# Optimization experiments

Measured on AMD Instinct MI355X. Metric: run time of the kernel, lower is better.

The kernel has to match this reference:

```python
import jax, jax.numpy as jnp
import numpy as np

B, T, D, H = 4, 2048, 1024, 2048   # batch, seq, d_model, moe_dim
E, S, K = 8, 2, 2                   # routed experts, shared experts, top_k


def setup_inputs() -> dict:
    key = jax.random.key(0)
    ks = jax.random.split(key, 10)
    s = 0.02  # init scale
    return {
        "x": jax.random.normal(ks[0], (B, T, D), jnp.float32),
        "gate_w": jax.random.normal(ks[1], (D, E), jnp.float32) * s,
        "gate_b": jnp.zeros((E,), jnp.float32),
        # routed experts, stacked over expert axis
        "rw1": jax.random.normal(ks[2], (E, D, H), jnp.float32) * s,
        "rb1": jnp.zeros((E, H), jnp.float32),
        "rw2": jax.random.normal(ks[3], (E, D, H), jnp.float32) * s,
        "rb2": jnp.zeros((E, H), jnp.float32),
        "rw3": jax.random.normal(ks[4], (E, H, D), jnp.float32) * s,
        "rb3": jnp.zeros((E, D), jnp.float32),
        # shared experts, stacked
        "sw1": jax.random.normal(ks[5], (S, D, H), jnp.float32) * s,
        "sb1": jnp.zeros((S, H), jnp.float32),
        "sw2": jax.random.normal(ks[6], (S, D, H), jnp.float32) * s,
        "sb2": jnp.zeros((S, H), jnp.float32),
        "sw3": jax.random.normal(ks[7], (S, H, D), jnp.float32) * s,
        "sb3": jnp.zeros((S, D), jnp.float32),
    }


def _swiglu_stacked(x, w1, b1, w2, b2, w3, b3):
    # x: (B,T,D); w1/w2: (N,D,H); w3: (N,H,D) -> out: (N,B,T,D)
    p1 = jnp.einsum('btd,ndh->nbth', x, w1) + b1[:, None, None, :]
    p2 = jnp.einsum('btd,ndh->nbth', x, w2) + b2[:, None, None, :]
    glu = jax.nn.silu(p1) * p2
    return jnp.einsum('nbth,nhd->nbtd', glu, w3) + b3[:, None, None, :]


def reference(x, gate_w, gate_b, rw1, rb1, rw2, rb2, rw3, rb3,
              sw1, sb1, sw2, sb2, sw3, sb3):
    # Gate: softmax over all routed experts, then top-k (no renormalization)
    scores = jax.nn.softmax(x @ gate_w + gate_b, axis=-1)      # (B,T,E)
    weights, indices = jax.lax.top_k(scores, K)                # (B,T,K)

    # Routed experts: compute all experts densely (same math as the naive
    # masked-dense torch loop), then gather top-k outputs per token.
    routed_all = _swiglu_stacked(x, rw1, rb1, rw2, rb2, rw3, rb3)  # (E,B,T,D)
    out_bted = jnp.transpose(routed_all, (1, 2, 0, 3))             # (B,T,E,D)
    gathered = jnp.take_along_axis(out_bted, indices[..., None], axis=2)  # (B,T,K,D)
    routed = jnp.sum(weights[..., None] * gathered, axis=2)        # (B,T,D)

    # Shared experts: mean over shared experts
    shared = _swiglu_stacked(x, sw1, sb1, sw2, sb2, sw3, sb3).mean(axis=0)

    return shared + routed
```

## Files before the change

kernel.cpp:

```cpp
#include <hip/hip_runtime.h>
#include <math.h>

#define TOKENS   8192
#define DMODEL   1024
#define HDIM     2048
#define NEXP     8
#define NSH      2
#define NGRP     10
#define R_ROUTED 16384
#define R_TOTAL  32768

typedef float  f32x4  __attribute__((ext_vector_type(4)));
typedef __bf16 bf16x8 __attribute__((ext_vector_type(8)));
typedef unsigned short u16x8 __attribute__((ext_vector_type(8)));

typedef __attribute__((address_space(1))) const void as1_void;
typedef __attribute__((address_space(3))) void as3_void;
#define GLOAD16(g, l) __builtin_amdgcn_global_load_lds((as1_void*)(g), (as3_void*)(l), 16, 0, 0)

__device__ __forceinline__ unsigned short f2bf(float f) {
  unsigned int u = __float_as_uint(f);
  u += 0x7fffu + ((u >> 16) & 1u);
  return (unsigned short)(u >> 16);
}
__device__ __forceinline__ float bf2f(unsigned short u) {
  return __uint_as_float(((unsigned int)u) << 16);
}


__global__ __launch_bounds__(256) void convert_x_kernel(const float* __restrict__ x,
                                                        unsigned short* __restrict__ xb) {
  int i = blockIdx.x * blockDim.x + threadIdx.x;
  const float4 v = reinterpret_cast<const float4*>(x)[i];
  ushort4 o;
  o.x = f2bf(v.x); o.y = f2bf(v.y); o.z = f2bf(v.z); o.w = f2bf(v.w);
  reinterpret_cast<ushort4*>(xb)[i] = o;
}

__global__ __launch_bounds__(256) void transpose_cvt64_kernel(const float* __restrict__ src,
                                                              unsigned short* __restrict__ dst,
                                                              int R, int C) {
  __shared__ float tile[64][65];
  const size_t mat = blockIdx.z;
  src += mat * (size_t)R * C;
  dst += mat * (size_t)R * C;
  const int c0 = blockIdx.x * 64, r0 = blockIdx.y * 64;
  const int tid = threadIdx.x;
  const int tx = tid & 15, ty = tid >> 4;
  #pragma unroll
  for (int rr = 0; rr < 4; ++rr) {
    const int row = ty + rr * 16;
    const float4 v = *reinterpret_cast<const float4*>(&src[(size_t)(r0 + row) * C + c0 + tx * 4]);
    tile[row][tx * 4 + 0] = v.x;
    tile[row][tx * 4 + 1] = v.y;
    tile[row][tx * 4 + 2] = v.z;
    tile[row][tx * 4 + 3] = v.w;
  }
  __syncthreads();
  const int oc = tid >> 2, og = tid & 3;
  u16x8 u0, u1;
  #pragma unroll
  for (int e = 0; e < 8; ++e) u0[e] = f2bf(tile[og * 16 + e][oc]);
  #pragma unroll
  for (int e = 0; e < 8; ++e) u1[e] = f2bf(tile[og * 16 + 8 + e][oc]);
  unsigned short* dp = &dst[(size_t)(c0 + oc) * R + r0 + og * 16];
  *reinterpret_cast<u16x8*>(dp) = u0;
  *reinterpret_cast<u16x8*>(dp + 8) = u1;
}


__global__ __launch_bounds__(64) void gate_kernel(const float* __restrict__ x,
                                                  const float* __restrict__ gw,
                                                  const float* __restrict__ gb,
                                                  int* __restrict__ topk_idx,
                                                  float* __restrict__ topk_w,
                                                  int* __restrict__ counts) {
  const int t = blockIdx.x;
  const int lane = threadIdx.x;
  const float* xr = x + (size_t)t * DMODEL;
  float acc[NEXP];
  #pragma unroll
  for (int e = 0; e < NEXP; ++e) acc[e] = 0.f;
  for (int d = lane; d < DMODEL; d += 64) {
    const float xv = xr[d];
    const float* g = gw + (size_t)d * NEXP;
    #pragma unroll
    for (int e = 0; e < NEXP; ++e) acc[e] += xv * g[e];
  }
  #pragma unroll
  for (int e = 0; e < NEXP; ++e) {
    float v = acc[e];
    v += __shfl_down(v, 32); v += __shfl_down(v, 16); v += __shfl_down(v, 8);
    v += __shfl_down(v, 4);  v += __shfl_down(v, 2);  v += __shfl_down(v, 1);
    acc[e] = v;
  }
  if (lane == 0) {
    float p[NEXP];
    float mx = -1e30f;
    #pragma unroll
    for (int e = 0; e < NEXP; ++e) { acc[e] += gb[e]; mx = fmaxf(mx, acc[e]); }
    float s = 0.f;
    #pragma unroll
    for (int e = 0; e < NEXP; ++e) { p[e] = expf(acc[e] - mx); s += p[e]; }
    const float inv = 1.f / s;
    #pragma unroll
    for (int e = 0; e < NEXP; ++e) p[e] *= inv;
    int i1 = 0; float v1 = p[0];
    #pragma unroll
    for (int e = 1; e < NEXP; ++e) if (p[e] > v1) { v1 = p[e]; i1 = e; }
    int i2 = -1; float v2 = -1e30f;
    #pragma unroll
    for (int e = 0; e < NEXP; ++e) if (e != i1 && p[e] > v2) { v2 = p[e]; i2 = e; }
    topk_idx[t * 2 + 0] = i1; topk_w[t * 2 + 0] = v1;
    topk_idx[t * 2 + 1] = i2; topk_w[t * 2 + 1] = v2;
    atomicAdd(&counts[i1], 1);
    atomicAdd(&counts[i2], 1);
  }
}

__global__ void offs_kernel(const int* __restrict__ counts, int* __restrict__ offs) {
  if (threadIdx.x == 0 && blockIdx.x == 0) {
    int cum = 0;
    for (int e = 0; e < NEXP; ++e) { offs[e] = cum; cum += counts[e]; }
    offs[8] = R_ROUTED;
    offs[9] = R_ROUTED + TOKENS;
    offs[10] = R_TOTAL;
  }
}

__global__ __launch_bounds__(256) void scatter_kernel(const int* __restrict__ topk_idx,
                                                      const int* __restrict__ offs,
                                                      int* __restrict__ cursors,
                                                      int* __restrict__ row_token,
                                                      int* __restrict__ tok_rows) {
  const int t = blockIdx.x * blockDim.x + threadIdx.x;
  if (t >= TOKENS) return;
  #pragma unroll
  for (int k = 0; k < 2; ++k) {
    const int e = topk_idx[t * 2 + k];
    const int pos = atomicAdd(&cursors[e], 1);
    const int r = offs[e] + pos;
    row_token[r] = t;
    tok_rows[t * 2 + k] = r;
  }
  row_token[R_ROUTED + t] = t;
  row_token[R_ROUTED + TOKENS + t] = t;
}


__global__ __launch_bounds__(256, 3) void gemm1_kernel(
    const unsigned short* __restrict__ xb,
    const unsigned short* __restrict__ w1t,
    const unsigned short* __restrict__ w2t,
    const float* __restrict__ rb1, const float* __restrict__ sb1,
    const float* __restrict__ rb2, const float* __restrict__ sb2,
    const int* __restrict__ offs,
    const int* __restrict__ row_token,
    unsigned short* __restrict__ glu) {
  const int g = blockIdx.z;
  const int off_g = offs[g];
  const int n_g = offs[g + 1] - off_g;
  const int m0 = blockIdx.x * 128;
  if (m0 >= n_g) return;
  const int n0 = blockIdx.y * 64;

  __shared__ __align__(16) unsigned short Abuf[128 * 64];
  __shared__ __align__(16) unsigned short B1buf[64 * 64];
  __shared__ __align__(16) unsigned short B2buf[64 * 64];

  const int tid = threadIdx.x;
  const int lane = tid & 63;
  const int wid = tid >> 6;
  const int wm = wid >> 1, wn = wid & 1;
  const int l15 = lane & 15, kq = lane >> 4;

  const unsigned short* w1g = w1t + (size_t)g * HDIM * DMODEL;
  const unsigned short* w2g = w2t + (size_t)g * HDIM * DMODEL;

  const unsigned short* srcA[4]; int dA[4];
  #pragma unroll
  for (int r = 0; r < 4; ++r) {
    const int chunk = r * 256 + tid, row = chunk >> 3, j = chunk & 7;
    int ar = m0 + row; if (ar > n_g - 1) ar = n_g - 1;
    srcA[r] = xb + (size_t)row_token[off_g + ar] * DMODEL + ((j ^ (row & 7)) << 3);
    dA[r] = (r * 256 + (tid & ~63)) << 3;
  }
  const unsigned short* srcB1[2]; const unsigned short* srcB2[2]; int dB[2];
  #pragma unroll
  for (int r = 0; r < 2; ++r) {
    const int chunk = r * 256 + tid, row = chunk >> 3, j = chunk & 7;
    const size_t o = (size_t)(n0 + row) * DMODEL + ((j ^ (row & 7)) << 3);
    srcB1[r] = w1g + o; srcB2[r] = w2g + o;
    dB[r] = (r * 256 + (tid & ~63)) << 3;
  }

  f32x4 acc1[4][2], acc2[4][2];
  const f32x4 zero = {0.f, 0.f, 0.f, 0.f};
  #pragma unroll
  for (int i = 0; i < 4; ++i)
    #pragma unroll
    for (int j = 0; j < 2; ++j) { acc1[i][j] = zero; acc2[i][j] = zero; }

  for (int k0 = 0; k0 < DMODEL; k0 += 64) {
    __syncthreads();
    #pragma unroll
    for (int r = 0; r < 4; ++r) GLOAD16(srcA[r] + k0, &Abuf[dA[r]]);
    #pragma unroll
    for (int r = 0; r < 2; ++r) {
      GLOAD16(srcB1[r] + k0, &B1buf[dB[r]]);
      GLOAD16(srcB2[r] + k0, &B2buf[dB[r]]);
    }
    __syncthreads();
    #pragma unroll
    for (int ks = 0; ks < 2; ++ks) {
      const int kc = ks * 4 + kq;
      bf16x8 a[4], p[2], q[2];
      #pragma unroll
      for (int mi = 0; mi < 4; ++mi) {
        const int row = wm * 64 + mi * 16 + l15;
        a[mi] = *reinterpret_cast<const bf16x8*>(&Abuf[row * 64 + ((kc ^ (row & 7)) << 3)]);
      }
      #pragma unroll
      for (int ni = 0; ni < 2; ++ni) {
        const int row = wn * 32 + ni * 16 + l15;
        const int ko = (kc ^ (row & 7)) << 3;
        p[ni] = *reinterpret_cast<const bf16x8*>(&B1buf[row * 64 + ko]);
        q[ni] = *reinterpret_cast<const bf16x8*>(&B2buf[row * 64 + ko]);
      }
      #pragma unroll
      for (int mi = 0; mi < 4; ++mi)
        #pragma unroll
        for (int ni = 0; ni < 2; ++ni) {
          acc1[mi][ni] = __builtin_amdgcn_mfma_f32_16x16x32_bf16(a[mi], p[ni], acc1[mi][ni], 0, 0, 0);
          acc2[mi][ni] = __builtin_amdgcn_mfma_f32_16x16x32_bf16(a[mi], q[ni], acc2[mi][ni], 0, 0, 0);
        }
    }
  }

  const float* b1p = (g < NEXP) ? (rb1 + (size_t)g * HDIM) : (sb1 + (size_t)(g - NEXP) * HDIM);
  const float* b2p = (g < NEXP) ? (rb2 + (size_t)g * HDIM) : (sb2 + (size_t)(g - NEXP) * HDIM);

  #pragma unroll
  for (int mi = 0; mi < 4; ++mi) {
    #pragma unroll
    for (int r = 0; r < 4; ++r) {
      const int m = m0 + wm * 64 + mi * 16 + kq * 4 + r;
      if (m < n_g) {
        #pragma unroll
        for (int ni = 0; ni < 2; ++ni) {
          const int n = n0 + wn * 32 + ni * 16 + l15;
          const float x1 = acc1[mi][ni][r] + b1p[n];
          const float x2 = acc2[mi][ni][r] + b2p[n];
          glu[(size_t)(off_g + m) * HDIM + n] = f2bf((x1 / (1.f + expf(-x1))) * x2);
        }
      }
    }
  }
}


__global__ __launch_bounds__(256, 3) void gemm2_kernel(
    const unsigned short* __restrict__ glu,
    const unsigned short* __restrict__ w3t,
    const float* __restrict__ rb3, const float* __restrict__ sb3,
    const int* __restrict__ offs,
    unsigned short* __restrict__ y) {
  const int g = blockIdx.z;
  const int off_g = offs[g];
  const int n_g = offs[g + 1] - off_g;
  const int m0 = blockIdx.x * 128;
  if (m0 >= n_g) return;
  const int n0 = blockIdx.y * 128;

  __shared__ __align__(16) unsigned short Abuf[128 * 64];
  __shared__ __align__(16) unsigned short Bbuf[128 * 64];

  const int tid = threadIdx.x;
  const int lane = tid & 63;
  const int wid = tid >> 6;
  const int wm = wid >> 1, wn = wid & 1;
  const int l15 = lane & 15, kq = lane >> 4;

  const unsigned short* w3g = w3t + (size_t)g * DMODEL * HDIM;

  const unsigned short* srcA[4]; const unsigned short* srcB[4]; int dAB[4];
  #pragma unroll
  for (int r = 0; r < 4; ++r) {
    const int chunk = r * 256 + tid, row = chunk >> 3, j = chunk & 7;
    int ar = m0 + row; if (ar > n_g - 1) ar = n_g - 1;
    srcA[r] = glu + (size_t)(off_g + ar) * HDIM + ((j ^ (row & 7)) << 3);
    srcB[r] = w3g + (size_t)(n0 + row) * HDIM + ((j ^ (row & 7)) << 3);
    dAB[r] = (r * 256 + (tid & ~63)) << 3;
  }

  f32x4 acc[4][4];
  const f32x4 zero = {0.f, 0.f, 0.f, 0.f};
  #pragma unroll
  for (int i = 0; i < 4; ++i)
    #pragma unroll
    for (int j = 0; j < 4; ++j) acc[i][j] = zero;

  for (int k0 = 0; k0 < HDIM; k0 += 64) {
    __syncthreads();
    #pragma unroll
    for (int r = 0; r < 4; ++r) {
      GLOAD16(srcA[r] + k0, &Abuf[dAB[r]]);
      GLOAD16(srcB[r] + k0, &Bbuf[dAB[r]]);
    }
    __syncthreads();
    #pragma unroll
    for (int ks = 0; ks < 2; ++ks) {
      const int kc = ks * 4 + kq;
      bf16x8 a[4], b[4];
      #pragma unroll
      for (int mi = 0; mi < 4; ++mi) {
        const int row = wm * 64 + mi * 16 + l15;
        a[mi] = *reinterpret_cast<const bf16x8*>(&Abuf[row * 64 + ((kc ^ (row & 7)) << 3)]);
      }
      #pragma unroll
      for (int ni = 0; ni < 4; ++ni) {
        const int row = wn * 64 + ni * 16 + l15;
        b[ni] = *reinterpret_cast<const bf16x8*>(&Bbuf[row * 64 + ((kc ^ (row & 7)) << 3)]);
      }
      #pragma unroll
      for (int mi = 0; mi < 4; ++mi)
        #pragma unroll
        for (int ni = 0; ni < 4; ++ni)
          acc[mi][ni] = __builtin_amdgcn_mfma_f32_16x16x32_bf16(a[mi], b[ni], acc[mi][ni], 0, 0, 0);
    }
  }

  const float* b3p = (g < NEXP) ? (rb3 + (size_t)g * DMODEL) : (sb3 + (size_t)(g - NEXP) * DMODEL);

  #pragma unroll
  for (int mi = 0; mi < 4; ++mi) {
    #pragma unroll
    for (int r = 0; r < 4; ++r) {
      const int m = m0 + wm * 64 + mi * 16 + kq * 4 + r;
      if (m < n_g) {
        unsigned short* yrow = y + (size_t)(off_g + m) * DMODEL;
        #pragma unroll
        for (int ni = 0; ni < 4; ++ni) {
          const int n = n0 + wn * 64 + ni * 16 + l15;
          yrow[n] = f2bf(acc[mi][ni][r] + b3p[n]);
        }
      }
    }
  }
}


__global__ __launch_bounds__(256) void reduce_kernel(const unsigned short* __restrict__ y,
                                                     const int* __restrict__ tok_rows,
                                                     const float* __restrict__ topk_w,
                                                     float* __restrict__ out) {
  const int t = blockIdx.x * 2 + (threadIdx.x >> 7);
  const int col = (threadIdx.x & 127) * 8;
  const int r0 = tok_rows[t * 2 + 0], r1 = tok_rows[t * 2 + 1];
  const float w0 = topk_w[t * 2 + 0], w1 = topk_w[t * 2 + 1];

  float o[8];
  #pragma unroll
  for (int e = 0; e < 8; ++e) o[e] = 0.f;
  auto addrow = [&](const unsigned short* p, float w) {
    const u16x8 v = *reinterpret_cast<const u16x8*>(p);
    #pragma unroll
    for (int e = 0; e < 8; ++e) o[e] += w * bf2f(v[e]);
  };
  addrow(y + (size_t)r0 * DMODEL + col, w0);
  addrow(y + (size_t)r1 * DMODEL + col, w1);
  addrow(y + (size_t)(R_ROUTED + t) * DMODEL + col, 0.5f);
  addrow(y + (size_t)(R_ROUTED + TOKENS + t) * DMODEL + col, 0.5f);

  float4* op = reinterpret_cast<float4*>(out + (size_t)t * DMODEL + col);
  op[0] = make_float4(o[0], o[1], o[2], o[3]);
  op[1] = make_float4(o[4], o[5], o[6], o[7]);
}


extern "C" void kernel_launch(void* const* d_in, const int* in_sizes, int n_in,
                              void* d_out, int out_size, void* d_ws, size_t ws_size,
                              hipStream_t stream) {
  const float* x      = (const float*)d_in[0];
  const float* gate_w = (const float*)d_in[1];
  const float* gate_b = (const float*)d_in[2];
  const float* rw1    = (const float*)d_in[3];
  const float* rb1    = (const float*)d_in[4];
  const float* rw2    = (const float*)d_in[5];
  const float* rb2    = (const float*)d_in[6];
  const float* rw3    = (const float*)d_in[7];
  const float* rb3    = (const float*)d_in[8];
  const float* sw1    = (const float*)d_in[9];
  const float* sb1    = (const float*)d_in[10];
  const float* sw2    = (const float*)d_in[11];
  const float* sb2    = (const float*)d_in[12];
  const float* sw3    = (const float*)d_in[13];
  const float* sb3    = (const float*)d_in[14];
  float* out = (float*)d_out;

  const size_t XB_OFF   = 0;
  const size_t W1T_OFF  = XB_OFF  + (size_t)TOKENS * DMODEL * 2;
  const size_t W2T_OFF  = W1T_OFF + (size_t)NGRP * HDIM * DMODEL * 2;
  const size_t W3T_OFF  = W2T_OFF + (size_t)NGRP * HDIM * DMODEL * 2;
  const size_t GLU_OFF  = W3T_OFF + (size_t)NGRP * DMODEL * HDIM * 2;
  const size_t Y_OFF    = W1T_OFF;
  const size_t RTOK_OFF = GLU_OFF + (size_t)R_TOTAL * HDIM * 2;
  const size_t TKI_OFF  = RTOK_OFF + (size_t)R_TOTAL * 4;
  const size_t TKW_OFF  = TKI_OFF + (size_t)TOKENS * 2 * 4;
  const size_t TRW_OFF  = TKW_OFF + (size_t)TOKENS * 2 * 4;
  const size_t META_OFF = TRW_OFF + (size_t)TOKENS * 2 * 4;
  const size_t NEED     = META_OFF + 256;
  if (ws_size < NEED) return;

  char* ws = (char*)d_ws;
  unsigned short* xb   = (unsigned short*)(ws + XB_OFF);
  unsigned short* w1t  = (unsigned short*)(ws + W1T_OFF);
  unsigned short* w2t  = (unsigned short*)(ws + W2T_OFF);
  unsigned short* w3t  = (unsigned short*)(ws + W3T_OFF);
  unsigned short* glu  = (unsigned short*)(ws + GLU_OFF);
  unsigned short* yy   = (unsigned short*)(ws + Y_OFF);
  int*   row_token = (int*)(ws + RTOK_OFF);
  int*   topk_idx  = (int*)(ws + TKI_OFF);
  float* topk_w    = (float*)(ws + TKW_OFF);
  int*   tok_rows  = (int*)(ws + TRW_OFF);
  int*   counts    = (int*)(ws + META_OFF);
  int*   offs      = counts + 16;
  int*   cursors   = counts + 32;

  hipMemsetAsync(counts, 0, 192, stream);

  convert_x_kernel<<<TOKENS * DMODEL / 4 / 256, 256, 0, stream>>>(x, xb);

  transpose_cvt64_kernel<<<dim3(HDIM / 64, DMODEL / 64, NEXP), 256, 0, stream>>>(rw1, w1t, DMODEL, HDIM);
  transpose_cvt64_kernel<<<dim3(HDIM / 64, DMODEL / 64, NSH), 256, 0, stream>>>(
      sw1, w1t + (size_t)NEXP * HDIM * DMODEL, DMODEL, HDIM);
  transpose_cvt64_kernel<<<dim3(HDIM / 64, DMODEL / 64, NEXP), 256, 0, stream>>>(rw2, w2t, DMODEL, HDIM);
  transpose_cvt64_kernel<<<dim3(HDIM / 64, DMODEL / 64, NSH), 256, 0, stream>>>(
      sw2, w2t + (size_t)NEXP * HDIM * DMODEL, DMODEL, HDIM);
  transpose_cvt64_kernel<<<dim3(DMODEL / 64, HDIM / 64, NEXP), 256, 0, stream>>>(rw3, w3t, HDIM, DMODEL);
  transpose_cvt64_kernel<<<dim3(DMODEL / 64, HDIM / 64, NSH), 256, 0, stream>>>(
      sw3, w3t + (size_t)NEXP * DMODEL * HDIM, HDIM, DMODEL);

  gate_kernel<<<TOKENS, 64, 0, stream>>>(x, gate_w, gate_b, topk_idx, topk_w, counts);
  offs_kernel<<<1, 64, 0, stream>>>(counts, offs);
  scatter_kernel<<<TOKENS / 256, 256, 0, stream>>>(topk_idx, offs, cursors,
                                                   row_token, tok_rows);

  gemm1_kernel<<<dim3(TOKENS / 128, HDIM / 64, NGRP), 256, 0, stream>>>(
      xb, w1t, w2t, rb1, sb1, rb2, sb2, offs, row_token, glu);
  gemm2_kernel<<<dim3(TOKENS / 128, DMODEL / 128, NGRP), 256, 0, stream>>>(
      glu, w3t, rb3, sb3, offs, yy);
  reduce_kernel<<<TOKENS / 2, 256, 0, stream>>>(yy, tok_rows, topk_w, out);
}
```

Measured before the change: 1.040 ms.

## Merge weight-transpose launches, fuse x conversion into gate, use 8-wave GEMM blocks

```diff
diff --git a/kernel.cpp b/kernel.cpp
--- a/kernel.cpp
+++ b/kernel.cpp
@@ -27,23 +27,20 @@
   return __uint_as_float(((unsigned int)u) << 16);
 }
 
-
-__global__ __launch_bounds__(256) void convert_x_kernel(const float* __restrict__ x,
-                                                        unsigned short* __restrict__ xb) {
-  int i = blockIdx.x * blockDim.x + threadIdx.x;
-  const float4 v = reinterpret_cast<const float4*>(x)[i];
-  ushort4 o;
-  o.x = f2bf(v.x); o.y = f2bf(v.y); o.z = f2bf(v.z); o.w = f2bf(v.w);
-  reinterpret_cast<ushort4*>(xb)[i] = o;
-}
-
-__global__ __launch_bounds__(256) void transpose_cvt64_kernel(const float* __restrict__ src,
-                                                              unsigned short* __restrict__ dst,
-                                                              int R, int C) {
+__global__ __launch_bounds__(256) void transpose_cvt64_kernel(
+    const float* __restrict__ s0, const float* __restrict__ s1,
+    const float* __restrict__ s2, const float* __restrict__ s3,
+    unsigned short* __restrict__ dst, int R, int C, int n0, int n1) {
   __shared__ float tile[64][65];
-  const size_t mat = blockIdx.z;
-  src += mat * (size_t)R * C;
-  dst += mat * (size_t)R * C;
+  const int z = blockIdx.z;
+  const size_t msz = (size_t)R * C;
+  const float* src;
+  if (z < n0) src = s0 + (size_t)z * msz;
+  else if (z < n0 + n1) src = s1 + (size_t)(z - n0) * msz;
+  else if (z < n0 + n1 + 8) src = s2 + (size_t)(z - n0 - n1) * msz;
+  else src = s3 + (size_t)(z - n0 - n1 - 8) * msz;
+  unsigned short* d = dst + (size_t)z * msz;
+
   const int c0 = blockIdx.x * 64, r0 = blockIdx.y * 64;
   const int tid = threadIdx.x;
   const int tx = tid & 15, ty = tid >> 4;
@@ -63,29 +60,40 @@
   for (int e = 0; e < 8; ++e) u0[e] = f2bf(tile[og * 16 + e][oc]);
   #pragma unroll
   for (int e = 0; e < 8; ++e) u1[e] = f2bf(tile[og * 16 + 8 + e][oc]);
-  unsigned short* dp = &dst[(size_t)(c0 + oc) * R + r0 + og * 16];
+  unsigned short* dp = &d[(size_t)(c0 + oc) * R + r0 + og * 16];
   *reinterpret_cast<u16x8*>(dp) = u0;
   *reinterpret_cast<u16x8*>(dp + 8) = u1;
 }
 
 
-__global__ __launch_bounds__(64) void gate_kernel(const float* __restrict__ x,
-                                                  const float* __restrict__ gw,
-                                                  const float* __restrict__ gb,
-                                                  int* __restrict__ topk_idx,
-                                                  float* __restrict__ topk_w,
-                                                  int* __restrict__ counts) {
-  const int t = blockIdx.x;
-  const int lane = threadIdx.x;
+__global__ __launch_bounds__(256) void gate_kernel(const float* __restrict__ x,
+                                                   const float* __restrict__ gw,
+                                                   const float* __restrict__ gb,
+                                                   int* __restrict__ topk_idx,
+                                                   float* __restrict__ topk_w,
+                                                   int* __restrict__ counts,
+                                                   unsigned short* __restrict__ xb) {
+  const int t = blockIdx.x * 4 + (threadIdx.x >> 6);
+  const int lane = threadIdx.x & 63;
   const float* xr = x + (size_t)t * DMODEL;
+  unsigned short* xbr = xb + (size_t)t * DMODEL;
   float acc[NEXP];
   #pragma unroll
   for (int e = 0; e < NEXP; ++e) acc[e] = 0.f;
-  for (int d = lane; d < DMODEL; d += 64) {
-    const float xv = xr[d];
-    const float* g = gw + (size_t)d * NEXP;
-    #pragma unroll
-    for (int e = 0; e < NEXP; ++e) acc[e] += xv * g[e];
+  #pragma unroll
+  for (int j = 0; j < 4; ++j) {
+    const int d = j * 256 + lane * 4;
+    const float4 v = *reinterpret_cast<const float4*>(&xr[d]);
+    ushort4 o;
+    o.x = f2bf(v.x); o.y = f2bf(v.y); o.z = f2bf(v.z); o.w = f2bf(v.w);
+    *reinterpret_cast<ushort4*>(&xbr[d]) = o;
+    #pragma unroll
+    for (int q = 0; q < 4; ++q) {
+      const float xv = (&v.x)[q];
+      const float* g = gw + (size_t)(d + q) * NEXP;
+      #pragma unroll
+      for (int e = 0; e < NEXP; ++e) acc[e] += xv * g[e];
+    }
   }
   #pragma unroll
   for (int e = 0; e < NEXP; ++e) {
@@ -148,7 +156,7 @@
 }
 
 
-__global__ __launch_bounds__(256, 3) void gemm1_kernel(
+__global__ __launch_bounds__(512, 4) void gemm1_kernel(
     const unsigned short* __restrict__ xb,
     const unsigned short* __restrict__ w1t,
     const unsigned short* __restrict__ w2t,
@@ -171,95 +179,84 @@
   const int tid = threadIdx.x;
   const int lane = tid & 63;
   const int wid = tid >> 6;
-  const int wm = wid >> 1, wn = wid & 1;
+  const int wm = wid >> 2, wn = wid & 3;
   const int l15 = lane & 15, kq = lane >> 4;
 
   const unsigned short* w1g = w1t + (size_t)g * HDIM * DMODEL;
   const unsigned short* w2g = w2t + (size_t)g * HDIM * DMODEL;
 
-  const unsigned short* srcA[4]; int dA[4];
-  #pragma unroll
-  for (int r = 0; r < 4; ++r) {
-    const int chunk = r * 256 + tid, row = chunk >> 3, j = chunk & 7;
+  const unsigned short* srcA[2]; int dA[2];
+  #pragma unroll
+  for (int r = 0; r < 2; ++r) {
+    const int chunk = r * 512 + tid, row = chunk >> 3, j = chunk & 7;
     int ar = m0 + row; if (ar > n_g - 1) ar = n_g - 1;
     srcA[r] = xb + (size_t)row_token[off_g + ar] * DMODEL + ((j ^ (row & 7)) << 3);
-    dA[r] = (r * 256 + (tid & ~63)) << 3;
-  }
-  const unsigned short* srcB1[2]; const unsigned short* srcB2[2]; int dB[2];
-  #pragma unroll
-  for (int r = 0; r < 2; ++r) {
-    const int chunk = r * 256 + tid, row = chunk >> 3, j = chunk & 7;
+    dA[r] = (r * 512 + (tid & ~63)) << 3;
+  }
+  const unsigned short* srcB1; const unsigned short* srcB2; int dB;
+  {
+    const int row = tid >> 3, j = tid & 7;
     const size_t o = (size_t)(n0 + row) * DMODEL + ((j ^ (row & 7)) << 3);
-    srcB1[r] = w1g + o; srcB2[r] = w2g + o;
-    dB[r] = (r * 256 + (tid & ~63)) << 3;
-  }
-
-  f32x4 acc1[4][2], acc2[4][2];
+    srcB1 = w1g + o; srcB2 = w2g + o;
+    dB = (tid & ~63) << 3;
+  }
+
+  f32x4 acc1[4], acc2[4];
   const f32x4 zero = {0.f, 0.f, 0.f, 0.f};
   #pragma unroll
-  for (int i = 0; i < 4; ++i)
-    #pragma unroll
-    for (int j = 0; j < 2; ++j) { acc1[i][j] = zero; acc2[i][j] = zero; }
+  for (int i = 0; i < 4; ++i) { acc1[i] = zero; acc2[i] = zero; }
 
   for (int k0 = 0; k0 < DMODEL; k0 += 64) {
     __syncthreads();
-    #pragma unroll
-    for (int r = 0; r < 4; ++r) GLOAD16(srcA[r] + k0, &Abuf[dA[r]]);
-    #pragma unroll
-    for (int r = 0; r < 2; ++r) {
-      GLOAD16(srcB1[r] + k0, &B1buf[dB[r]]);
-      GLOAD16(srcB2[r] + k0, &B2buf[dB[r]]);
-    }
+    GLOAD16(srcA[0] + k0, &Abuf[dA[0]]);
+    GLOAD16(srcA[1] + k0, &Abuf[dA[1]]);
+    GLOAD16(srcB1 + k0, &B1buf[dB]);
+    GLOAD16(srcB2 + k0, &B2buf[dB]);
     __syncthreads();
     #pragma unroll
     for (int ks = 0; ks < 2; ++ks) {
       const int kc = ks * 4 + kq;
-      bf16x8 a[4], p[2], q[2];
+      bf16x8 a[4], p, q;
       #pragma unroll
       for (int mi = 0; mi < 4; ++mi) {
         const int row = wm * 64 + mi * 16 + l15;
         a[mi] = *reinterpret_cast<const bf16x8*>(&Abuf[row * 64 + ((kc ^ (row & 7)) << 3)]);
       }
-      #pragma unroll
-      for (int ni = 0; ni < 2; ++ni) {
-        const int row = wn * 32 + ni * 16 + l15;
+      {
+        const int row = wn * 16 + l15;
         const int ko = (kc ^ (row & 7)) << 3;
-        p[ni] = *reinterpret_cast<const bf16x8*>(&B1buf[row * 64 + ko]);
-        q[ni] = *reinterpret_cast<const bf16x8*>(&B2buf[row * 64 + ko]);
-      }
-      #pragma unroll
-      for (int mi = 0; mi < 4; ++mi)
-        #pragma unroll
-        for (int ni = 0; ni < 2; ++ni) {
-          acc1[mi][ni] = __builtin_amdgcn_mfma_f32_16x16x32_bf16(a[mi], p[ni], acc1[mi][ni], 0, 0, 0);
-          acc2[mi][ni] = __builtin_amdgcn_mfma_f32_16x16x32_bf16(a[mi], q[ni], acc2[mi][ni], 0, 0, 0);
-        }
+        p = *reinterpret_cast<const bf16x8*>(&B1buf[row * 64 + ko]);
+        q = *reinterpret_cast<const bf16x8*>(&B2buf[row * 64 + ko]);
+      }
+      #pragma unroll
+      for (int mi = 0; mi < 4; ++mi) {
+        acc1[mi] = __builtin_amdgcn_mfma_f32_16x16x32_bf16(a[mi], p, acc1[mi], 0, 0, 0);
+        acc2[mi] = __builtin_amdgcn_mfma_f32_16x16x32_bf16(a[mi], q, acc2[mi], 0, 0, 0);
+      }
     }
   }
 
   const float* b1p = (g < NEXP) ? (rb1 + (size_t)g * HDIM) : (sb1 + (size_t)(g - NEXP) * HDIM);
   const float* b2p = (g < NEXP) ? (rb2 + (size_t)g * HDIM) : (sb2 + (size_t)(g - NEXP) * HDIM);
 
+  const int n = n0 + wn * 16 + l15;
+  const float bb1 = b1p[n], bb2 = b2p[n];
   #pragma unroll
   for (int mi = 0; mi < 4; ++mi) {
     #pragma unroll
     for (int r = 0; r < 4; ++r) {
       const int m = m0 + wm * 64 + mi * 16 + kq * 4 + r;
       if (m < n_g) {
-        #pragma unroll
-        for (int ni = 0; ni < 2; ++ni) {
-          const int n = n0 + wn * 32 + ni * 16 + l15;
-          const float x1 = acc1[mi][ni][r] + b1p[n];
-          const float x2 = acc2[mi][ni][r] + b2p[n];
-          glu[(size_t)(off_g + m) * HDIM + n] = f2bf((x1 / (1.f + expf(-x1))) * x2);
-        }
+        const float x1 = acc1[mi][r] + bb1;
+        const float x2 = acc2[mi][r] + bb2;
+        glu[(size_t)(off_g + m) * HDIM + n] = f2bf((x1 / (1.f + expf(-x1))) * x2);
       }
     }
   }
 }
 
 
-__global__ __launch_bounds__(256, 3) void gemm2_kernel(
+__global__ __launch_bounds__(512, 4) void gemm2_kernel(
     const unsigned short* __restrict__ glu,
     const unsigned short* __restrict__ w3t,
     const float* __restrict__ rb3, const float* __restrict__ sb3,
@@ -278,54 +275,53 @@
   const int tid = threadIdx.x;
   const int lane = tid & 63;
   const int wid = tid >> 6;
-  const int wm = wid >> 1, wn = wid & 1;
+  const int wm = wid >> 2, wn = wid & 3;
   const int l15 = lane & 15, kq = lane >> 4;
 
   const unsigned short* w3g = w3t + (size_t)g * DMODEL * HDIM;
 
-  const unsigned short* srcA[4]; const unsigned short* srcB[4]; int dAB[4];
-  #pragma unroll
-  for (int r = 0; r < 4; ++r) {
-    const int chunk = r * 256 + tid, row = chunk >> 3, j = chunk & 7;
+  const unsigned short* srcA[2]; const unsigned short* srcB[2]; int dAB[2];
+  #pragma unroll
+  for (int r = 0; r < 2; ++r) {
+    const int chunk = r * 512 + tid, row = chunk >> 3, j = chunk & 7;
     int ar = m0 + row; if (ar > n_g - 1) ar = n_g - 1;
     srcA[r] = glu + (size_t)(off_g + ar) * HDIM + ((j ^ (row & 7)) << 3);
     srcB[r] = w3g + (size_t)(n0 + row) * HDIM + ((j ^ (row & 7)) << 3);
-    dAB[r] = (r * 256 + (tid & ~63)) << 3;
-  }
-
-  f32x4 acc[4][4];
+    dAB[r] = (r * 512 + (tid & ~63)) << 3;
+  }
+
+  f32x4 acc[4][2];
   const f32x4 zero = {0.f, 0.f, 0.f, 0.f};
   #pragma unroll
   for (int i = 0; i < 4; ++i)
     #pragma unroll
-    for (int j = 0; j < 4; ++j) acc[i][j] = zero;
+    for (int j = 0; j < 2; ++j) acc[i][j] = zero;
 
   for (int k0 = 0; k0 < HDIM; k0 += 64) {
     __syncthreads();
-    #pragma unroll
-    for (int r = 0; r < 4; ++r) {
-      GLOAD16(srcA[r] + k0, &Abuf[dAB[r]]);
-      GLOAD16(srcB[r] + k0, &Bbuf[dAB[r]]);
-    }
+    GLOAD16(srcA[0] + k0, &Abuf[dAB[0]]);
+    GLOAD16(srcA[1] + k0, &Abuf[dAB[1]]);
+    GLOAD16(srcB[0] + k0, &Bbuf[dAB[0]]);
+    GLOAD16(srcB[1] + k0, &Bbuf[dAB[1]]);
     __syncthreads();
     #pragma unroll
     for (int ks = 0; ks < 2; ++ks) {
       const int kc = ks * 4 + kq;
-      bf16x8 a[4], b[4];
+      bf16x8 a[4], b[2];
       #pragma unroll
       for (int mi = 0; mi < 4; ++mi) {
         const int row = wm * 64 + mi * 16 + l15;
         a[mi] = *reinterpret_cast<const bf16x8*>(&Abuf[row * 64 + ((kc ^ (row & 7)) << 3)]);
       }
       #pragma unroll
-      for (int ni = 0; ni < 4; ++ni) {
-        const int row = wn * 64 + ni * 16 + l15;
+      for (int ni = 0; ni < 2; ++ni) {
+        const int row = wn * 32 + ni * 16 + l15;
         b[ni] = *reinterpret_cast<const bf16x8*>(&Bbuf[row * 64 + ((kc ^ (row & 7)) << 3)]);
       }
       #pragma unroll
       for (int mi = 0; mi < 4; ++mi)
         #pragma unroll
-        for (int ni = 0; ni < 4; ++ni)
+        for (int ni = 0; ni < 2; ++ni)
           acc[mi][ni] = __builtin_amdgcn_mfma_f32_16x16x32_bf16(a[mi], b[ni], acc[mi][ni], 0, 0, 0);
     }
   }
@@ -340,8 +336,8 @@
       if (m < n_g) {
         unsigned short* yrow = y + (size_t)(off_g + m) * DMODEL;
         #pragma unroll
-        for (int ni = 0; ni < 4; ++ni) {
-          const int n = n0 + wn * 64 + ni * 16 + l15;
+        for (int ni = 0; ni < 2; ++ni) {
+          const int n = n0 + wn * 32 + ni * 16 + l15;
           yrow[n] = f2bf(acc[mi][ni][r] + b3p[n]);
         }
       }
@@ -400,8 +396,7 @@
 
   const size_t XB_OFF   = 0;
   const size_t W1T_OFF  = XB_OFF  + (size_t)TOKENS * DMODEL * 2;
-  const size_t W2T_OFF  = W1T_OFF + (size_t)NGRP * HDIM * DMODEL * 2;
-  const size_t W3T_OFF  = W2T_OFF + (size_t)NGRP * HDIM * DMODEL * 2;
+  const size_t W3T_OFF  = W1T_OFF + (size_t)2 * NGRP * HDIM * DMODEL * 2;
   const size_t GLU_OFF  = W3T_OFF + (size_t)NGRP * DMODEL * HDIM * 2;
   const size_t Y_OFF    = W1T_OFF;
   const size_t RTOK_OFF = GLU_OFF + (size_t)R_TOTAL * HDIM * 2;
@@ -415,7 +410,7 @@
   char* ws = (char*)d_ws;
   unsigned short* xb   = (unsigned short*)(ws + XB_OFF);
   unsigned short* w1t  = (unsigned short*)(ws + W1T_OFF);
-  unsigned short* w2t  = (unsigned short*)(ws + W2T_OFF);
+  unsigned short* w2t  = w1t + (size_t)NGRP * HDIM * DMODEL;
   unsigned short* w3t  = (unsigned short*)(ws + W3T_OFF);
   unsigned short* glu  = (unsigned short*)(ws + GLU_OFF);
   unsigned short* yy   = (unsigned short*)(ws + Y_OFF);
@@ -429,26 +424,19 @@
 
   hipMemsetAsync(counts, 0, 192, stream);
 
-  convert_x_kernel<<<TOKENS * DMODEL / 4 / 256, 256, 0, stream>>>(x, xb);
-
-  transpose_cvt64_kernel<<<dim3(HDIM / 64, DMODEL / 64, NEXP), 256, 0, stream>>>(rw1, w1t, DMODEL, HDIM);
-  transpose_cvt64_kernel<<<dim3(HDIM / 64, DMODEL / 64, NSH), 256, 0, stream>>>(
-      sw1, w1t + (size_t)NEXP * HDIM * DMODEL, DMODEL, HDIM);
-  transpose_cvt64_kernel<<<dim3(HDIM / 64, DMODEL / 64, NEXP), 256, 0, stream>>>(rw2, w2t, DMODEL, HDIM);
-  transpose_cvt64_kernel<<<dim3(HDIM / 64, DMODEL / 64, NSH), 256, 0, stream>>>(
-      sw2, w2t + (size_t)NEXP * HDIM * DMODEL, DMODEL, HDIM);
-  transpose_cvt64_kernel<<<dim3(DMODEL / 64, HDIM / 64, NEXP), 256, 0, stream>>>(rw3, w3t, HDIM, DMODEL);
-  transpose_cvt64_kernel<<<dim3(DMODEL / 64, HDIM / 64, NSH), 256, 0, stream>>>(
-      sw3, w3t + (size_t)NEXP * DMODEL * HDIM, HDIM, DMODEL);
-
-  gate_kernel<<<TOKENS, 64, 0, stream>>>(x, gate_w, gate_b, topk_idx, topk_w, counts);
+  transpose_cvt64_kernel<<<dim3(HDIM / 64, DMODEL / 64, 20), 256, 0, stream>>>(
+      rw1, sw1, rw2, sw2, w1t, DMODEL, HDIM, 8, 2);
+  transpose_cvt64_kernel<<<dim3(DMODEL / 64, HDIM / 64, 10), 256, 0, stream>>>(
+      rw3, sw3, rw3, rw3, w3t, HDIM, DMODEL, 8, 2);
+
+  gate_kernel<<<TOKENS / 4, 256, 0, stream>>>(x, gate_w, gate_b, topk_idx, topk_w, counts, xb);
   offs_kernel<<<1, 64, 0, stream>>>(counts, offs);
   scatter_kernel<<<TOKENS / 256, 256, 0, stream>>>(topk_idx, offs, cursors,
                                                    row_token, tok_rows);
 
-  gemm1_kernel<<<dim3(TOKENS / 128, HDIM / 64, NGRP), 256, 0, stream>>>(
+  gemm1_kernel<<<dim3(TOKENS / 128, HDIM / 64, NGRP), 512, 0, stream>>>(
       xb, w1t, w2t, rb1, sb1, rb2, sb2, offs, row_token, glu);
-  gemm2_kernel<<<dim3(TOKENS / 128, DMODEL / 128, NGRP), 256, 0, stream>>>(
+  gemm2_kernel<<<dim3(TOKENS / 128, DMODEL / 128, NGRP), 512, 0, stream>>>(
       glu, w3t, rb3, sb3, offs, yy);
   reduce_kernel<<<TOKENS / 2, 256, 0, stream>>>(yy, tok_rows, topk_w, out);
 }
```

Result: slower. 1.131 ms (+8.7%).
